# Kernel optimization log

Measured on AMD Instinct MI355X. Metric: run time of the kernel, lower is better.

The kernel has to match this reference:

```python
import jax, jax.numpy as jnp
import numpy as np

N_FFT = 1024
HOP = 256
WIN_LENGTH = 1024
B = 16
T = 480000


def setup_inputs() -> dict:
    key = jax.random.key(0)
    k1, k2 = jax.random.split(key)
    x = jax.random.normal(k1, (B, T), dtype=jnp.float32)
    window = jax.random.uniform(k2, (WIN_LENGTH,), dtype=jnp.float32)
    return {"x": x, "window": window}


def _dft_kernels(window):
    # pad window to n_fft if needed (here win_length == n_fft)
    if WIN_LENGTH < N_FFT:
        pl = (N_FFT - WIN_LENGTH) // 2
        window = jnp.pad(window, (pl, N_FFT - WIN_LENGTH - pl))
    n_freq = N_FFT // 2 + 1
    k = jnp.arange(n_freq, dtype=jnp.float32)[:, None]   # [F,1]
    n = jnp.arange(N_FFT, dtype=jnp.float32)[None, :]    # [1,N]
    basis = (2.0 * np.pi / N_FFT) * k * n                # [F,N]
    cos_k = jnp.cos(basis) * window[None, :]
    sin_k = -jnp.sin(basis) * window[None, :]
    return cos_k, sin_k


def reference(x, window):
    pad = N_FFT // 2
    xp = jnp.pad(x, ((0, 0), (pad, pad)), mode="reflect")  # center=True, reflect
    n_frames = (xp.shape[1] - N_FFT) // HOP + 1
    # frame extraction: [n_frames, n_fft] gather indices (strided windows)
    idx = jnp.arange(n_frames)[:, None] * HOP + jnp.arange(N_FFT)[None, :]
    frames = xp[:, idx]                                   # [B, n_frames, n_fft]
    cos_k, sin_k = _dft_kernels(window)                   # [F, n_fft]
    real = jnp.einsum("btn,fn->btf", frames, cos_k)        # [B, n_frames, F]
    imag = jnp.einsum("btn,fn->btf", frames, sin_k)
    return jnp.stack([real, imag], axis=-1)               # [B, n_frames, F, 2]
```

## Files before the change

kernel.cpp:

```cpp
#include <hip/hip_runtime.h>

#define BATCH     16
#define T_LEN     480000
#define PAD       512
#define TPAD      481024
#define HOP       256
#define NFRAMES   1876
#define FRPAD     1920
#define NOUTROW   1026
#define KTOT      1024
#define NCOLS     1152

#define BM        128
#define BN        128
#define BK        32
#define ACH       4352
#define XPSTRIDE  493568

typedef __attribute__((ext_vector_type(8))) short short8;
typedef __attribute__((ext_vector_type(4))) float floatx4;

__device__ __forceinline__ unsigned short f2bf(float f) {
  union { float f; unsigned int u; } v; v.f = f;
  unsigned int u = v.u;
  return (unsigned short)((u + 0x7FFFu + ((u >> 16) & 1u)) >> 16);
}

__global__ __launch_bounds__(256) void build_xp(const float* __restrict__ x,
                                                unsigned short* __restrict__ xp) {
  const int i = blockIdx.x * 256 + threadIdx.x;
  const int b = blockIdx.y;
  unsigned short v = 0;
  if (i < TPAD) {
    int j = i - PAD;
    if (j < 0) j = -j;
    if (j >= T_LEN) j = 2 * T_LEN - 2 - j;
    v = f2bf(x[(size_t)b * T_LEN + j]);
  }
  xp[(size_t)b * XPSTRIDE + i] = v;
}

__global__ __launch_bounds__(256) void build_bmat(const float* __restrict__ win,
                                                  unsigned short* __restrict__ bm) {
  const int k = blockIdx.x * 256 + threadIdx.x;
  const int j = blockIdx.y;
  unsigned short o = 0;
  if (j < NOUTROW) {
    const int f = j >> 1;
    const int r = (f * k) & (KTOT - 1);
    const float ang = (float)r * 6.1359231515e-3f;
    const float c = __cosf(ang), s = __sinf(ang);
    const float v = (j & 1) ? -s : c;
    o = f2bf(v * win[k]);
  }
  bm[(size_t)j * KTOT + k] = o;
}

__global__ __launch_bounds__(256, 2) void stft_gemm(const unsigned short* __restrict__ xp,
                                                    const unsigned short* __restrict__ bmat,
                                                    float* __restrict__ out) {
  __shared__ unsigned short As[ACH * 8];
  __shared__ unsigned short Bs[BN * BK];

  const int tid  = threadIdx.x;
  const int lane = tid & 63;
  const int wv   = tid >> 6;
  const int wr   = wv >> 1, wc = wv & 1;
  const int bx   = blockIdx.x;
  const int b    = bx / 15;
  const int t0   = (bx - b * 15) * BM;
  const int j0   = blockIdx.y * BN;
  const int L    = lane & 15;
  const int quad = lane >> 4;

  const unsigned short* abase = xp + (size_t)b * XPSTRIDE + (size_t)t0 * HOP;

#pragma unroll
  for (int r = 0; r < ACH / 256; ++r) {
    const int ci = r * 256 + tid;
    const int s  = ci ^ ((ci >> 5) & 7);
    __builtin_amdgcn_global_load_lds(
        (const __attribute__((address_space(1))) void*)(abase + s * 8),
        (__attribute__((address_space(3))) void*)((char*)As + ci * 16),
        16, 0, 0);
  }

  const unsigned short* bsrc[2];
#pragma unroll
  for (int p = 0; p < 2; ++p) {
    const int ci  = p * 256 + tid;
    const int col = ci >> 2, c = ci & 3;
    bsrc[p] = bmat + (size_t)(j0 + col) * KTOT + c * 8;
  }

  int sbase[4];
  const unsigned short* blds[4];
#pragma unroll
  for (int t = 0; t < 4; ++t) {
    const int ml = wr * 64 + t * 16 + L;
    sbase[t] = 32 * ml + quad;
    const int n = wc * 64 + t * 16 + L;
    blds[t] = &Bs[n * BK + quad * 8];
  }

  floatx4 acc[4][4] = {};

  for (int k0 = 0; k0 < KTOT; k0 += BK) {
#pragma unroll
    for (int p = 0; p < 2; ++p) {
      const int ci = p * 256 + tid;
      __builtin_amdgcn_global_load_lds(
          (const __attribute__((address_space(1))) void*)(bsrc[p] + k0),
          (__attribute__((address_space(3))) void*)((char*)Bs + ci * 16),
          16, 0, 0);
    }
    __syncthreads();

    short8 af[4], bf[4];
    const int kc = k0 >> 3;
#pragma unroll
    for (int t = 0; t < 4; ++t) {
      const int s = sbase[t] + kc;
      const int p = s ^ ((s >> 5) & 7);
      af[t] = *(const short8*)&As[p * 8];
      bf[t] = *(const short8*)blds[t];
    }
#pragma unroll
    for (int ti = 0; ti < 4; ++ti)
#pragma unroll
      for (int tj = 0; tj < 4; ++tj)
        acc[ti][tj] = __builtin_amdgcn_mfma_f32_16x16x32_bf16(
            af[ti], bf[tj], acc[ti][tj], 0, 0, 0);
    __syncthreads();
  }

#pragma unroll
  for (int ti = 0; ti < 4; ++ti) {
    const int tb = t0 + wr * 64 + ti * 16 + quad * 4;
#pragma unroll
    for (int tj = 0; tj < 4; ++tj) {
      const int gj = j0 + wc * 64 + tj * 16 + L;
      if (gj < NOUTROW) {
#pragma unroll
        for (int i = 0; i < 4; ++i) {
          const int t = tb + i;
          if (t < NFRAMES)
            out[(size_t)(b * NFRAMES + t) * NOUTROW + gj] = acc[ti][tj][i];
        }
      }
    }
  }
}

extern "C" void kernel_launch(void* const* d_in, const int* in_sizes, int n_in,
                              void* d_out, int out_size, void* d_ws, size_t ws_size,
                              hipStream_t stream) {
  const float* x   = (const float*)d_in[0];
  const float* win = (const float*)d_in[1];
  float* out = (float*)d_out;

  unsigned short* xp   = (unsigned short*)d_ws;
  unsigned short* bmat = xp + (size_t)BATCH * XPSTRIDE;

  build_xp  <<<dim3(XPSTRIDE / 256, BATCH), 256, 0, stream>>>(x, xp);
  build_bmat<<<dim3(KTOT / 256, NCOLS),     256, 0, stream>>>(win, bmat);
  stft_gemm <<<dim3(BATCH * (FRPAD / BM), NCOLS / BN), 256, 0, stream>>>(xp, bmat, out);
}
```

Measured before the change: 250.7 us.

## Load A fragments from global directly and double-buffer B tiles in LDS

Drops the large LDS-resident A panel and has each lane load its A fragments straight from global memory (L2/L1 reuse across overlapping frames), with register prefetch of the next k-slice. B tiles are now double-buffered in LDS so the next tile's async load overlaps the current MFMA work. The smaller LDS footprint allows the launch bound to rise to 4 blocks per CU for more occupancy. The cost is more global/L1 traffic for A, whose overlapping frames are re-read by many lanes, and extra register pressure under the tighter launch bound.

After: 318.6 us. 1.27x slower.

```diff
diff --git a/kernel.cpp b/kernel.cpp
--- a/kernel.cpp
+++ b/kernel.cpp
@@ -14,7 +14,6 @@
 #define BM        128
 #define BN        128
 #define BK        32
-#define ACH       4352
 #define XPSTRIDE  493568
 
 typedef __attribute__((ext_vector_type(8))) short short8;
@@ -56,11 +55,11 @@
   bm[(size_t)j * KTOT + k] = o;
 }
 
-__global__ __launch_bounds__(256, 2) void stft_gemm(const unsigned short* __restrict__ xp,
+__global__ __launch_bounds__(256, 4) void stft_gemm(const unsigned short* __restrict__ xp,
                                                     const unsigned short* __restrict__ bmat,
                                                     float* __restrict__ out) {
-  __shared__ unsigned short As[ACH * 8];
-  __shared__ unsigned short Bs[BN * BK];
+  __shared__ unsigned short Bs0[BN * BK];
+  __shared__ unsigned short Bs1[BN * BK];
 
   const int tid  = threadIdx.x;
   const int lane = tid & 63;
@@ -73,64 +72,73 @@
   const int L    = lane & 15;
   const int quad = lane >> 4;
 
-  const unsigned short* abase = xp + (size_t)b * XPSTRIDE + (size_t)t0 * HOP;
-
+  const unsigned short* arow[4];
 #pragma unroll
-  for (int r = 0; r < ACH / 256; ++r) {
-    const int ci = r * 256 + tid;
-    const int s  = ci ^ ((ci >> 5) & 7);
-    __builtin_amdgcn_global_load_lds(
-        (const __attribute__((address_space(1))) void*)(abase + s * 8),
-        (__attribute__((address_space(3))) void*)((char*)As + ci * 16),
-        16, 0, 0);
+  for (int t = 0; t < 4; ++t) {
+    const int row = t0 + wr * 64 + t * 16 + L;
+    arow[t] = xp + (size_t)b * XPSTRIDE + (size_t)row * HOP + quad * 8;
   }
 
   const unsigned short* bsrc[2];
 #pragma unroll
   for (int p = 0; p < 2; ++p) {
-    const int ci  = p * 256 + tid;
-    const int col = ci >> 2, c = ci & 3;
-    bsrc[p] = bmat + (size_t)(j0 + col) * KTOT + c * 8;
+    const int ci = p * 256 + tid;
+    bsrc[p] = bmat + (size_t)(j0 + (ci >> 2)) * KTOT + (ci & 3) * 8;
   }
 
-  int sbase[4];
-  const unsigned short* blds[4];
+  int boff[4];
 #pragma unroll
-  for (int t = 0; t < 4; ++t) {
-    const int ml = wr * 64 + t * 16 + L;
-    sbase[t] = 32 * ml + quad;
-    const int n = wc * 64 + t * 16 + L;
-    blds[t] = &Bs[n * BK + quad * 8];
-  }
+  for (int t = 0; t < 4; ++t) boff[t] = (wc * 64 + t * 16 + L) * BK + quad * 8;
 
+  short8 af[4], afn[4];
   floatx4 acc[4][4] = {};
 
-  for (int k0 = 0; k0 < KTOT; k0 += BK) {
+  auto stage = [&](unsigned short* dst, int kk) {
 #pragma unroll
     for (int p = 0; p < 2; ++p) {
       const int ci = p * 256 + tid;
       __builtin_amdgcn_global_load_lds(
-          (const __attribute__((address_space(1))) void*)(bsrc[p] + k0),
-          (__attribute__((address_space(3))) void*)((char*)Bs + ci * 16),
+          (const __attribute__((address_space(1))) void*)(bsrc[p] + kk),
+          (__attribute__((address_space(3))) void*)((char*)dst + ci * 16),
           16, 0, 0);
     }
-    __syncthreads();
-
-    short8 af[4], bf[4];
-    const int kc = k0 >> 3;
+  };
+  auto aload = [&](int kk) {
 #pragma unroll
-    for (int t = 0; t < 4; ++t) {
-      const int s = sbase[t] + kc;
-      const int p = s ^ ((s >> 5) & 7);
-      af[t] = *(const short8*)&As[p * 8];
-      bf[t] = *(const short8*)blds[t];
-    }
+    for (int t = 0; t < 4; ++t) afn[t] = *(const short8*)(arow[t] + kk);
+  };
+  auto compute = [&](const unsigned short* bb) {
+    short8 bf[4];
+#pragma unroll
+    for (int t = 0; t < 4; ++t) bf[t] = *(const short8*)&bb[boff[t]];
 #pragma unroll
     for (int ti = 0; ti < 4; ++ti)
 #pragma unroll
       for (int tj = 0; tj < 4; ++tj)
         acc[ti][tj] = __builtin_amdgcn_mfma_f32_16x16x32_bf16(
             af[ti], bf[tj], acc[ti][tj], 0, 0, 0);
+  };
+
+#pragma unroll
+  for (int t = 0; t < 4; ++t) af[t] = *(const short8*)arow[t];
+  stage(Bs0, 0);
+  __syncthreads();
+
+  for (int k0 = 0; k0 < KTOT; k0 += 2 * BK) {
+    stage(Bs1, k0 + BK);
+    aload(k0 + BK);
+    compute(Bs0);
+#pragma unroll
+    for (int t = 0; t < 4; ++t) af[t] = afn[t];
+    __syncthreads();
+
+    const bool more = (k0 + 2 * BK) < KTOT;
+    if (more) { stage(Bs0, k0 + 2 * BK); aload(k0 + 2 * BK); }
+    compute(Bs1);
+    if (more) {
+#pragma unroll
+      for (int t = 0; t < 4; ++t) af[t] = afn[t];
+    }
     __syncthreads();
   }
 
```

## Double-buffer A and B tiles per K-step instead of preloading whole A strip

Applied to the files above, without the earlier changes.

Replaces the up-front load of the entire overlapping A strip into LDS (about 70KB) with per-K-step 128x32 A tiles that are streamed and double-buffered alongside the B tiles. The next stage is issued before the MFMAs on the current buffer, which lets global-to-LDS loads overlap compute. It also switches to an XOR swizzle of 16-byte chunks to avoid bank conflicts. The much smaller LDS footprint allows occupancy to rise from 2 to 3 blocks per CU. In exchange, A data shared between overlapping frames is now reloaded from global memory for every tile, so the kernel moves more bytes.

Result: no change. 246.6 us (-1.6%).

```diff
diff --git a/kernel.cpp b/kernel.cpp
--- a/kernel.cpp
+++ b/kernel.cpp
@@ -14,7 +14,6 @@
 #define BM        128
 #define BN        128
 #define BK        32
-#define ACH       4352
 #define XPSTRIDE  493568
 
 typedef __attribute__((ext_vector_type(8))) short short8;
@@ -56,11 +55,11 @@
   bm[(size_t)j * KTOT + k] = o;
 }
 
-__global__ __launch_bounds__(256, 2) void stft_gemm(const unsigned short* __restrict__ xp,
+__global__ __launch_bounds__(256, 3) void stft_gemm(const unsigned short* __restrict__ xp,
                                                     const unsigned short* __restrict__ bmat,
                                                     float* __restrict__ out) {
-  __shared__ unsigned short As[ACH * 8];
-  __shared__ unsigned short Bs[BN * BK];
+  __shared__ unsigned short As[2][BM * BK];
+  __shared__ unsigned short Bs[2][BN * BK];
 
   const int tid  = threadIdx.x;
   const int lane = tid & 63;
@@ -73,57 +72,55 @@
   const int L    = lane & 15;
   const int quad = lane >> 4;
 
-  const unsigned short* abase = xp + (size_t)b * XPSTRIDE + (size_t)t0 * HOP;
-
-#pragma unroll
-  for (int r = 0; r < ACH / 256; ++r) {
-    const int ci = r * 256 + tid;
-    const int s  = ci ^ ((ci >> 5) & 7);
-    __builtin_amdgcn_global_load_lds(
-        (const __attribute__((address_space(1))) void*)(abase + s * 8),
-        (__attribute__((address_space(3))) void*)((char*)As + ci * 16),
-        16, 0, 0);
-  }
-
+  const unsigned short* asrc[2];
   const unsigned short* bsrc[2];
 #pragma unroll
   for (int p = 0; p < 2; ++p) {
     const int ci  = p * 256 + tid;
-    const int col = ci >> 2, c = ci & 3;
-    bsrc[p] = bmat + (size_t)(j0 + col) * KTOT + c * 8;
+    const int row = ci >> 2;
+    const int c   = (ci & 3) ^ (row & 3);
+    asrc[p] = xp + (size_t)b * XPSTRIDE + (size_t)(t0 + row) * HOP + c * 8;
+    bsrc[p] = bmat + (size_t)(j0 + row) * KTOT + c * 8;
   }
 
-  int sbase[4];
-  const unsigned short* blds[4];
+  int aoff[4], boff[4];
 #pragma unroll
   for (int t = 0; t < 4; ++t) {
-    const int ml = wr * 64 + t * 16 + L;
-    sbase[t] = 32 * ml + quad;
+    const int m = wr * 64 + t * 16 + L;
+    aoff[t] = m * BK + (quad ^ (m & 3)) * 8;
     const int n = wc * 64 + t * 16 + L;
-    blds[t] = &Bs[n * BK + quad * 8];
+    boff[t] = n * BK + (quad ^ (n & 3)) * 8;
   }
 
   floatx4 acc[4][4] = {};
 
-  for (int k0 = 0; k0 < KTOT; k0 += BK) {
+  auto stage = [&](int buf, int kk) {
 #pragma unroll
     for (int p = 0; p < 2; ++p) {
       const int ci = p * 256 + tid;
       __builtin_amdgcn_global_load_lds(
-          (const __attribute__((address_space(1))) void*)(bsrc[p] + k0),
-          (__attribute__((address_space(3))) void*)((char*)Bs + ci * 16),
+          (const __attribute__((address_space(1))) void*)(asrc[p] + kk),
+          (__attribute__((address_space(3))) void*)((char*)As[buf] + ci * 16),
+          16, 0, 0);
+      __builtin_amdgcn_global_load_lds(
+          (const __attribute__((address_space(1))) void*)(bsrc[p] + kk),
+          (__attribute__((address_space(3))) void*)((char*)Bs[buf] + ci * 16),
           16, 0, 0);
     }
-    __syncthreads();
+  };
+
+  stage(0, 0);
+  __syncthreads();
+
+  for (int k0 = 0; k0 < KTOT; k0 += BK) {
+    const int buf = (k0 >> 5) & 1;
+    if (k0 + BK < KTOT) stage(buf ^ 1, k0 + BK);
 
     short8 af[4], bf[4];
-    const int kc = k0 >> 3;
 #pragma unroll
     for (int t = 0; t < 4; ++t) {
-      const int s = sbase[t] + kc;
-      const int p = s ^ ((s >> 5) & 7);
-      af[t] = *(const short8*)&As[p * 8];
-      bf[t] = *(const short8*)blds[t];
+      af[t] = *(const short8*)&As[buf][aoff[t]];
+      bf[t] = *(const short8*)&Bs[buf][boff[t]];
     }
 #pragma unroll
     for (int ti = 0; ti < 4; ++ti)
@@ -131,6 +128,7 @@
       for (int tj = 0; tj < 4; ++tj)
         acc[ti][tj] = __builtin_amdgcn_mfma_f32_16x16x32_bf16(
             af[ti], bf[tj], acc[ti][tj], 0, 0, 0);
+
     __syncthreads();
   }
 
```
